# Kernel tuning notes

Hardware: AMD Instinct MI355X
Metric: run time of the kernel (lower is better)

Reference implementation:

```python
import jax, jax.numpy as jnp
import numpy as np

WAY = 5
TEMPERATURE = 0.2
TEMPERATURE_ATTN = 5.0
BN_EPS = 1e-5


def bn_apply(x, p):
    # p: (4, C) = gamma, beta, running_mean, running_var (eval-mode BatchNorm)
    g, b, m, v = p[0], p[1], p[2], p[3]
    sh = (1, -1) + (1,) * (x.ndim - 2)
    return (x - m.reshape(sh)) * (g.reshape(sh) / jnp.sqrt(v.reshape(sh) + BN_EPS)) + b.reshape(sh)


def conv3d(x, w, pad):
    return jax.lax.conv_general_dilated(
        x, w, (1, 1, 1), [(pad[0], pad[0]), (pad[1], pad[1]), (pad[2], pad[2])],
        dimension_numbers=('NCDHW', 'OIDHW', 'NCDHW'))


def sepconv4d(x, conv2_w, bn2, conv1_w, bn1, proj_w, bnp):
    # x: (b, c, u, v, h, w). conv2: (k,k,1) kernel over (u,v); conv1: (1,k,k) over (h,w).
    b, c, u, v, h, w = x.shape
    y = x.reshape(b, c, u, v, h * w)
    y = bn_apply(conv3d(y, conv2_w, (1, 1, 0)), bn2)
    y = jax.nn.relu(y)
    y = y.reshape(b, c, u * v, h, w)
    y = bn_apply(conv3d(y, conv1_w, (0, 1, 1)), bn1)
    # 1x1 projection (pointwise over channels) + BN
    y = jnp.einsum('oc,bcxhw->boxhw', proj_w, y)
    y = bn_apply(y, bnp)
    return y.reshape(b, -1, u, v, h, w)


def cca(x, c1, c2):
    def branch(z):
        z = sepconv4d(z, *c1)
        z = jax.nn.relu(z)
        z = sepconv4d(z, *c2)
        return z
    perm = (0, 1, 4, 5, 2, 3)
    return branch(x) + jnp.transpose(branch(jnp.transpose(x, perm)), perm)


def gaussian_normalize(x, axis, eps=1e-5):
    m = jnp.mean(x, axis=axis, keepdims=True)
    v = jnp.var(x, axis=axis, keepdims=True, ddof=1)  # torch.var is unbiased
    return (x - m) / jnp.sqrt(v + eps)


def setup_inputs() -> dict:
    key = jax.random.key(0)
    ks = jax.random.split(key, 16)

    def bn_params(k, c):
        k1, k2, k3, k4 = jax.random.split(k, 4)
        g = 1.0 + 0.1 * jax.random.normal(k1, (c,), jnp.float32)
        b = 0.1 * jax.random.normal(k2, (c,), jnp.float32)
        m = 0.1 * jax.random.normal(k3, (c,), jnp.float32)
        v = 1.0 + 0.1 * jax.random.uniform(k4, (c,), jnp.float32)
        return jnp.stack([g, b, m, v])

    return {
        'spt': jax.random.normal(ks[0], (1, 5, 640, 10, 10), jnp.float32),
        'qry': jax.random.normal(ks[1], (75, 640, 10, 10), jnp.float32),
        'w_1x1': jax.random.normal(ks[2], (64, 640), jnp.float32) * 0.04,
        'bn_1x1': bn_params(ks[3], 64),
        'c1_conv2_w': jax.random.normal(ks[4], (1, 1, 3, 3, 1), jnp.float32) * 0.33,
        'c1_bn2': bn_params(ks[5], 1),
        'c1_conv1_w': jax.random.normal(ks[6], (1, 1, 1, 3, 3), jnp.float32) * 0.33,
        'c1_bn1': bn_params(ks[7], 1),
        'c1_proj_w': jax.random.normal(ks[8], (16, 1), jnp.float32),
        'c1_bnp': bn_params(ks[9], 16),
        'c2_conv2_w': jax.random.normal(ks[10], (16, 16, 3, 3, 1), jnp.float32) * 0.083,
        'c2_bn2': bn_params(ks[11], 16),
        'c2_conv1_w': jax.random.normal(ks[12], (16, 16, 1, 3, 3), jnp.float32) * 0.083,
        'c2_bn1': bn_params(ks[13], 16),
        'c2_proj_w': jax.random.normal(ks[14], (1, 16), jnp.float32) * 0.25,
        'c2_bnp': bn_params(ks[15], 1),
    }


def reference(spt, qry, w_1x1, bn_1x1,
              c1_conv2_w, c1_bn2, c1_conv1_w, c1_bn1, c1_proj_w, c1_bnp,
              c2_conv2_w, c2_bn2, c2_conv1_w, c2_bn1, c2_proj_w, c2_bnp):
    s = spt[0]                                   # (way, C, H, W)
    s = s - s.mean(axis=1, keepdims=True)        # normalize_feature
    q = qry - qry.mean(axis=1, keepdims=True)

    def cca1x1(x):
        y = jnp.einsum('oc,bchw->bohw', w_1x1, x)
        return jax.nn.relu(bn_apply(y, bn_1x1))

    sf = cca1x1(s)
    qf = cca1x1(q)
    sf = sf / jnp.maximum(jnp.linalg.norm(sf, axis=1, keepdims=True), 1e-8)
    qf = qf / jnp.maximum(jnp.linalg.norm(qf, axis=1, keepdims=True), 1e-8)

    # 4D correlation (avoids the repeat-induced 6D blowup of the original)
    corr = jnp.einsum('ncij,qckl->qnijkl', sf, qf)  # (Q, way, Hs, Ws, Hq, Wq)
    Q, way, Hs, Ws, Hq, Wq = corr.shape

    c1 = (c1_conv2_w, c1_bn2, c1_conv1_w, c1_bn1, c1_proj_w, c1_bnp)
    c2 = (c2_conv2_w, c2_bn2, c2_conv1_w, c2_bn1, c2_proj_w, c2_bnp)
    corr = cca(corr.reshape(Q * way, 1, Hs, Ws, Hq, Wq), c1, c2)

    corr_s = corr.reshape(Q, way, Hs * Ws, Hq, Wq)
    corr_q = corr.reshape(Q, way, Hs, Ws, Hq * Wq)
    corr_s = gaussian_normalize(corr_s, axis=2)
    corr_q = gaussian_normalize(corr_q, axis=4)
    corr_s = jax.nn.softmax(corr_s / TEMPERATURE_ATTN, axis=2).reshape(Q, way, Hs, Ws, Hq, Wq)
    corr_q = jax.nn.softmax(corr_q / TEMPERATURE_ATTN, axis=4).reshape(Q, way, Hs, Ws, Hq, Wq)

    attn_s = corr_s.sum(axis=(4, 5))             # (Q, way, Hs, Ws)
    attn_q = corr_q.sum(axis=(2, 3))             # (Q, way, Hq, Wq)

    spt_att = (attn_s[:, :, None] * s[None]).mean(axis=(-1, -2))       # (Q, way, C)
    qry_att = (attn_q[:, :, None] * q[:, None]).mean(axis=(-1, -2))    # (Q, way, C)
    qry_pooled = q.mean(axis=(-1, -2))                                  # (Q, C)

    num = jnp.sum(spt_att * qry_att, axis=-1)
    den = (jnp.maximum(jnp.linalg.norm(spt_att, axis=-1), 1e-8) *
           jnp.maximum(jnp.linalg.norm(qry_att, axis=-1), 1e-8))
    sim = (num / den) / TEMPERATURE
    return sim, qry_pooled
```

## Files before the change

### kernel.cpp

```cpp
#include <hip/hip_runtime.h>


#define NITEM 375

#define OFF_XTS 0
#define OFF_XTQ 160000
#define OFF_MP  2560000
#define OFF_SF  2568000
#define OFF_QF  2600000
#define OFF_RA  3080000
#define OFF_RB  6830000
#define OFF_PRM 10655000

#define PK2F 232
#define PK1F 1512
#define WSUMF 2792
#define SCVF 2856
#define SHVF 2920
#define PKWF 2984

#define Y1SLOT0  23680
#define Y1GAP3   3200
#define Y1SSTR3  35200
#define ZPB3     20480
#define Y2S3     129280
#define LDS_TOTAL3 161536

typedef float f4v __attribute__((ext_vector_type(4)));
typedef float f32x4 __attribute__((ext_vector_type(4)));
typedef _Float16 half8v __attribute__((ext_vector_type(8)));
typedef __fp16 fp16x2 __attribute__((ext_vector_type(2)));
typedef unsigned int u32x4 __attribute__((ext_vector_type(4)));
typedef unsigned int u32x2 __attribute__((ext_vector_type(2)));

__device__ __forceinline__ unsigned int pkrtz(float a, float b) {
  union { fp16x2 h; unsigned int u; } cv;
  cv.h = __builtin_amdgcn_cvt_pkrtz(a, b);
  return cv.u;
}

__global__ __launch_bounds__(256) void k_prep(
    const float* __restrict__ w1x1,  const float* __restrict__ bn1x1,
    const float* __restrict__ c1c2w, const float* __restrict__ c1bn2,
    const float* __restrict__ c1c1w, const float* __restrict__ c1bn1,
    const float* __restrict__ c1pj,  const float* __restrict__ c1bnp,
    const float* __restrict__ c2c2w, const float* __restrict__ c2bn2,
    const float* __restrict__ c2c1w, const float* __restrict__ c2bn1,
    const float* __restrict__ c2pj,  const float* __restrict__ c2bnp,
    float* __restrict__ prm)
{
  (void)w1x1; (void)bn1x1;
  const int t = threadIdx.x;
  const float eps = 1e-5f;

  for (int idx = t; idx < 144; idx += 256) {
    int ds = idx / 16, i = idx % 16;
    float spv = c2bnp[0] / sqrtf(c2bnp[3] + eps);
    float acc = 0.f;
    for (int o = 0; o < 16; ++o) {
      float s1 = c2bn1[o] / sqrtf(c2bn1[48 + o] + eps);
      acc += c2pj[o] * s1 * c2c1w[(o * 16 + i) * 9 + ds];
    }
    prm[idx] = spv * acc;
  }
  for (int i = t; i < 16; i += 256) {
    float s = c1bnp[i] / sqrtf(c1bnp[48 + i] + eps);
    prm[144 + i] = s * c1pj[i];
    prm[160 + i] = c1bnp[16 + i] - c1bnp[32 + i] * s;
  }
  for (int o = t; o < 16; o += 256) {
    float s = c2bn2[o] / sqrtf(c2bn2[48 + o] + eps);
    prm[176 + o] = s;
    prm[192 + o] = c2bn2[16 + o] - c2bn2[32 + o] * s;
  }
  for (int k = t; k < 9; k += 256) {
    prm[208 + k] = c1c2w[k];
    prm[217 + k] = c1c1w[k];
  }
  if (t == 0) {
    float S2 = c1bn2[0] / sqrtf(c1bn2[3] + eps);
    prm[226] = S2;
    prm[227] = c1bn2[1] - c1bn2[2] * S2;
    float S1 = c1bn1[0] / sqrtf(c1bn1[3] + eps);
    prm[228] = S1;
    prm[229] = c1bn1[1] - c1bn1[2] * S1;
    float spv = c2bnp[0] / sqrtf(c2bnp[3] + eps);
    float k0 = 0.f;
    for (int o = 0; o < 16; ++o) {
      float s1 = c2bn1[o] / sqrtf(c2bn1[48 + o] + eps);
      k0 += c2pj[o] * (c2bn1[16 + o] - c2bn1[32 + o] * s1);
    }
    prm[230] = spv * (k0 - c2bnp[2]) + c2bnp[1];
    prm[231] = 0.f;
  }
  __syncthreads();

  _Float16* pk2 = (_Float16*)(prm + PK2F);
  for (int idx = t; idx < 2560; idx += 256) {
    int c = idx >> 9, rem = idx & 511;
    int ln = rem >> 3, j = rem & 7;
    int o = ln & 15, qq = ln >> 4;
    int tap = 2 * c + (qq >> 1);
    int i = (qq & 1) * 8 + j;
    float v = (tap < 9) ? c2c2w[(o * 16 + i) * 9 + tap] : 0.f;
    pk2[idx] = (_Float16)v;
  }
  _Float16* pk1 = (_Float16*)(prm + PK1F);
  for (int idx = t; idx < 2560; idx += 256) {
    int c = idx >> 9, rem = idx & 511;
    int ln = rem >> 3, j = rem & 7;
    int m = ln & 15, qq = ln >> 4;
    int k = c * 32 + qq * 8 + j;
    int tp = k >> 4, i = k & 15;
    float v = (m == 0 && tp < 9) ? prm[tp * 16 + i] : 0.f;
    pk1[idx] = (_Float16)v;
  }
}

__global__ __launch_bounds__(256) void k_prepw(
    const float* __restrict__ w1x1, const float* __restrict__ bn1x1,
    float* __restrict__ prm)
{
  __shared__ float red[4];
  _Float16* pkw = (_Float16*)(prm + PKWF);
  const int t = threadIdx.x;
  const int base = blockIdx.x * 800;
  for (int r = t; r < 800; r += 256) {
    int idx = base + r;
    int fi = idx >> 9, rem = idx & 511;
    int ln = rem >> 3, j = rem & 7;
    int cc = fi / 10, r2 = fi - cc * 10;
    int mt = r2 >> 1, kk = r2 & 1;
    int m = mt * 16 + (ln & 15);
    int k = cc * 64 + kk * 32 + ((ln >> 4) & 3) * 8 + j;
    float v = (m < 64) ? w1x1[m * 640 + k] : (m == 64 ? 1.f : 0.f);
    pkw[idx] = (_Float16)v;
  }
  const int o = blockIdx.x;
  float s = 0.f;
  for (int c = t; c < 640; c += 256) s += w1x1[o * 640 + c];
  #pragma unroll
  for (int off = 32; off > 0; off >>= 1) s += __shfl_down(s, off);
  if ((t & 63) == 0) red[t >> 6] = s;
  __syncthreads();
  if (t == 0) {
    prm[WSUMF + o] = red[0] + red[1] + red[2] + red[3];
    float scv = bn1x1[o] / sqrtf(bn1x1[192 + o] + 1e-5f);
    prm[SCVF + o] = scv;
    prm[SHVF + o] = bn1x1[64 + o] - bn1x1[128 + o] * scv;
  }
}

__global__ __launch_bounds__(512) void k_feat(
    const float* __restrict__ spt, const float* __restrict__ qry,
    float* __restrict__ ws, float* __restrict__ out)
{
  __shared__ __align__(16) char POOL[2 * 16128];
  __shared__ __align__(16) float mrow[112];
  __shared__ __align__(16) float rn[112];
  __shared__ float CS[2][512];
  __shared__ float RS[640];
  __shared__ float msumL;

  const int b = blockIdx.x, t = threadIdx.x;
  const int lane = t & 63, wvv = t >> 6;
  const int n0 = lane & 15, qd = (lane >> 4) & 3;
  const float* src = (b < 5) ? spt + b * 64000 : qry + (b - 5) * 64000;
  unsigned int* xtg = (unsigned int*)(ws + ((b < 5) ? (OFF_XTS + b * 32000)
                                                    : (OFF_XTQ + (b - 5) * 32000)));
  const float* prm = ws + OFF_PRM;
  const _Float16* pkw = (const _Float16*)(prm + PKWF);

  for (int idx = t; idx < 864; idx += 512) {
    int bsel = idx / 432, r = idx - bsel * 432;
    ((unsigned int*)(POOL + bsel * 16128 + 100 * 144))[r] = 0u;
  }
  for (int u = t; u < 800; u += 512) {
    int cp = u / 25, p4 = u - cp * 25;
    const float* r0 = src + (2 * cp) * 100 + p4 * 4;
    f4v a = *(const f4v*)r0;
    f4v c1 = *(const f4v*)(r0 + 100);
    #pragma unroll
    for (int e = 0; e < 4; ++e)
      *(unsigned int*)((_Float16*)POOL + (p4 * 4 + e) * 72 + 2 * cp) = pkrtz(a[e], c1[e]);
  }
  __syncthreads();

  const int chp = t >> 3, part = t & 7;
  const int pLo = part * 13, pHi = (pLo + 13 < 100) ? pLo + 13 : 100;

  f32x4 acc[5];
  #pragma unroll
  for (int ti = 0; ti < 5; ++ti) { acc[ti][0]=0.f; acc[ti][1]=0.f; acc[ti][2]=0.f; acc[ti][3]=0.f; }

  for (int cc = 0; cc < 10; ++cc) {
    const int cur = cc & 1;
    const _Float16* Xc = (const _Float16*)(POOL + cur * 16128);
    _Float16* Xn = (_Float16*)(POOL + (cur ^ 1) * 16128);

    f4v pa[2], pc[2];
    if (cc < 9) {
      #pragma unroll
// ... 45 lines not shown
      #pragma unroll
      for (int k = 0; k < 8; ++k) s += CS[cur][t * 8 + k];
      RS[cc * 64 + t] = s;
    }
  }
  #pragma unroll
  for (int ti = 0; ti < 5; ++ti) {
    int idx = wvv + ti * 8; if (idx > 34) idx = 34;
    int mt = idx / 7, nt = idx - mt * 7;
    if (mt == 4 && qd == 0) {
      int p = nt * 16 + n0;
      mrow[p] = acc[ti][0] * (1.f / 640.f);
    }
  }
  __syncthreads();
  float* OUT = (float*)POOL;
  if (t == 0) { float s = 0.f; for (int p = 0; p < 100; ++p) s += mrow[p]; msumL = s; }
  #pragma unroll
  for (int ti = 0; ti < 5; ++ti) {
    int idx = wvv + ti * 8; if (idx > 34) idx = 34;
    int mt = idx / 7, nt = idx - mt * 7;
    if (mt < 4) {
      int p = nt * 16 + n0;
      if (p < 100) {
        float mp = mrow[p];
        #pragma unroll
        for (int r = 0; r < 4; ++r) {
          int o = mt * 16 + qd * 4 + r;
          float v = acc[ti][r] - prm[WSUMF + o] * mp;
          v = prm[SCVF + o] * v + prm[SHVF + o];
          OUT[o * 104 + p] = v > 0.f ? v : 0.f;
        }
      }
    }
  }
  __syncthreads();
  if (t < 100) {
    float s = 0.f;
    for (int o = 0; o < 64; ++o) { float v = OUT[o * 104 + t]; s += v * v; }
    float nr = sqrtf(s);
    rn[t] = 1.f / (nr > 1e-8f ? nr : 1e-8f);
    ws[OFF_MP + b * 100 + t] = mrow[t];
  }
  __syncthreads();
  {
    unsigned int* fg = (unsigned int*)((b < 5) ? (ws + OFF_SF) : (ws + OFF_QF))
                       + ((b < 5) ? b : (b - 5)) * 3584;
    for (int idx = t; idx < 3584; idx += 512) {
      const int jj = idx & 3;
      const int ln2 = (idx >> 2) & 63;
      const int fi = idx >> 8;
      const int kk = fi / 7, pt = fi - kk * 7;
      const int pos = pt * 16 + (ln2 & 15);
      const int c0 = kk * 32 + ((ln2 >> 4) & 3) * 8 + 2 * jj;
      float a = 0.f, bb = 0.f;
      if (pos < 100) {
        const float rv = rn[pos];
        a = OUT[c0 * 104 + pos] * rv;
        bb = OUT[(c0 + 1) * 104 + pos] * rv;
      }
      fg[idx] = pkrtz(a, bb);
    }
  }
  if (b >= 5) {
    const float msum = msumL;
    for (int gc = t; gc < 640; gc += 512)
      out[375 + (b - 5) * 640 + gc] = (RS[gc] - msum) * 0.01f;
  }
}

__global__ __launch_bounds__(1024) __attribute__((amdgpu_waves_per_eu(4, 4)))
void k_cca(float* __restrict__ ws)
{
  extern __shared__ char smem[];
  _Float16* T2h = (_Float16*)smem;
  float* T1   = (float*)(smem + 20480);
  float* CORR = (float*)(smem + 71680);

  const float* prm = ws + OFF_PRM;
  const int bid = blockIdx.x;
  const int it = bid >> 1, br = bid & 1;
  const int q = it / 5, n = it % 5;
  const int t = threadIdx.x;
  const int lane = t & 63, wv = t >> 6;
  const int n0 = lane & 15, qd = (lane >> 4) & 3;
  const int qh = qd >> 1, ih = qd & 1;

  const _Float16* pk2 = (const _Float16*)(prm + PK2F);
  const _Float16* pk1 = (const _Float16*)(prm + PK1F);
  half8v A2[5], A1[5];
  #pragma unroll
  for (int c = 0; c < 5; ++c) {
    A2[c] = *(const half8v*)(pk2 + c * 512 + lane * 8);
    A1[c] = *(const half8v*)(pk1 + c * 512 + lane * 8);
  }
  float sc2[4], bc2[4];
  #pragma unroll
  for (int r = 0; r < 4; ++r) { sc2[r] = prm[176 + qd * 4 + r]; bc2[r] = prm[192 + qd * 4 + r]; }

  const int d1E[5] = {-1,-1, 0, 0, 1}, d2E[5] = {-1, 1, 0,-1, 1};
  const int d1O[5] = {-1, 0, 0, 1, 0}, d2O[5] = { 0,-1, 1, 0, 0};

  int pp1[4], st1[4], addr2[4][5], posB[4];
  bool pv[4];
  #pragma unroll
  for (int ti = 0; ti < 4; ++ti) {
    int tile = wv + ti * 16; if (tile > 62) tile = 62;
    const int p = tile * 16 + n0;
    const int pcp = p < 1000 ? p : 999;
    pp1[ti] = pcp * 32 + ih * 16;
    st1[ti] = Y2S3 + p * 32 + qh * 16 + ih * 8;
    pv[ti] = (qd == 0) && (p < 1000);
    const int f2 = pcp / 100;
    const int s = pcp - f2 * 100;
    const int s1 = s / 10, s2 = s - s1 * 10;
    const bool rm = s1 > 0, rp = s1 < 9, cm = s2 > 0, cp2 = s2 < 9;
    const int b0 = Y2S3 + pcp * 32 + ih * 16;
    #pragma unroll
    for (int c = 0; c < 5; ++c) {
      const bool vE = (d1E[c] < 0 ? rm : (d1E[c] > 0 ? rp : true)) &&
                      (d2E[c] < 0 ? cm : (d2E[c] > 0 ? cp2 : true));
      const bool vO = (c == 4) ? false :
                      ((d1O[c] < 0 ? rm : (d1O[c] > 0 ? rp : true)) &&
                       (d2O[c] < 0 ? cm : (d2O[c] > 0 ? cp2 : true)));
      const bool v = qh ? vO : vE;
      const int D1c = (qh ? (d1O[c] * 10 + d2O[c]) : (d1E[c] * 10 + d2E[c]));
      addr2[ti][c] = v ? (b0 + D1c * 32) : ZPB3;
    }
    posB[ti] = br ? (s * 100 + f2) : (f2 * 100 + s);
  }
  const int posStride = br ? 10 : 1000;

  {
    const half8v* fS = (const half8v*)(ws + OFF_SF) + n * 896;
    const half8v* fQ = (const half8v*)(ws + OFF_QF) + q * 896;
    const half8v* FA = br ? fQ : fS;
    const half8v* FB = br ? fS : fQ;
    #pragma unroll
    for (int ti = 0; ti < 4; ++ti) {
      int T = wv + ti * 16; if (T > 48) T = 48;
      const int mt = T / 7, nt = T - mt * 7;
      half8v a0 = FA[mt * 64 + lane];
      half8v b0 = FB[nt * 64 + lane];
      half8v a1 = FA[(7 + mt) * 64 + lane];
      half8v b1 = FB[(7 + nt) * 64 + lane];
      f32x4 acc; acc[0]=0.f; acc[1]=0.f; acc[2]=0.f; acc[3]=0.f;
      acc = __builtin_amdgcn_mfma_f32_16x16x32_f16(a0, b0, acc, 0, 0, 0);
      acc = __builtin_amdgcn_mfma_f32_16x16x32_f16(a1, b1, acc, 0, 0, 0);
      const int s = nt * 16 + n0;
      if (s < 100) {
        const int s1a = s / 10;
        float* cp0 = CORR + s1a * 12 + (s - s1a * 10);
        const int r0 = mt * 16 + qd * 4;
        #pragma unroll
        for (int r = 0; r < 4; ++r)
          if (r0 + r < 100) cp0[(r0 + r) * 120] = acc[r];
      }
    }
  }
  __syncthreads();

  const float S2 = prm[226], B2 = prm[227], S1 = prm[228], B1 = prm[229];

  if (t < 600) {
    const int h = t / 300, r2 = t - h * 300;
    const int f2 = r2 / 30, r3 = r2 - f2 * 30;
    const int s1v = r3 / 3, s2q = r3 - s1v * 3;
    const int cb = s1v * 12 + s2q * 4;
    f4v outv[5];
    #pragma unroll
    for (int i = 0; i < 5; ++i) { outv[i][0]=0.f; outv[i][1]=0.f; outv[i][2]=0.f; outv[i][3]=0.f; }
    #pragma unroll
    for (int k = 0; k < 7; ++k) {
      const int nf1 = 5 * h - 1 + k;
      if ((unsigned)nf1 >= 10u) continue;
      #pragma unroll
      for (int dv = 0; dv < 3; ++dv) {
        const int nf2 = f2 + dv - 1;
        if ((unsigned)nf2 >= 10u) continue;
        f4v x = *(const f4v*)(CORR + (nf1 * 10 + nf2) * 120 + cb);
        #pragma unroll
        for (int du = 0; du < 3; ++du) {
          const int f1l = k - du;
          if (f1l < 0 || f1l > 4) continue;
          const float w = prm[208 + du * 3 + dv];
          #pragma unroll
          for (int e = 0; e < 4; ++e) outv[f1l][e] += w * x[e];
        }
      }
    }
    #pragma unroll
    for (int f1l = 0; f1l < 5; ++f1l) {
      const int f = (5 * h + f1l) * 10 + f2;
      f4v v;
      #pragma unroll
      for (int e = 0; e < 4; ++e) { float z = S2 * outv[f1l][e] + B2; v[e] = z > 0.f ? z : 0.f; }
      *(f4v*)(T1 + f * 120 + cb) = v;
    }
  }
  __syncthreads();

  if (t < 1000) {
    const int f = t / 10, s1 = t - (t / 10) * 10;
    const float* rowB = T1 + f * 120;
    f4v r[3][3];
    float w[3][3];
    #pragma unroll
    for (int dh = 0; dh < 3; ++dh) {
      int rr = s1 + dh - 1;
      bool okr = (unsigned)rr < 10u;
      int rc = rr < 0 ? 0 : (rr > 9 ? 9 : rr);
      const float* rp = rowB + rc * 12;
      r[dh][0] = *(const f4v*)(rp);
      r[dh][1] = *(const f4v*)(rp + 4);
      r[dh][2] = *(const f4v*)(rp + 8);
      #pragma unroll
      for (int dw = 0; dw < 3; ++dw) w[dh][dw] = okr ? prm[217 + dh * 3 + dw] : 0.f;
    }
    float o[10];
    #pragma unroll
    for (int s2 = 0; s2 < 10; ++s2) {
      float a = 0.f;
      #pragma unroll
      for (int dh = 0; dh < 3; ++dh)
        #pragma unroll
        for (int dw = 0; dw < 3; ++dw) {
          int col = s2 + dw - 1;
          if (col < 0 || col > 9) continue;
          a += w[dh][dw] * r[dh][col >> 2][col & 3];
        }
      o[s2] = a;
    }
    unsigned int* dst = (unsigned int*)((char*)T2h + (f * 100 + s1 * 10) * 2);
    #pragma unroll
    for (int k = 0; k < 5; ++k)
      dst[k] = pkrtz(S1 * o[2 * k] + B1, S1 * o[2 * k + 1] + B1);
  }
  __syncthreads();

  #define GEN_Y1(F1N)                                                          \
    if (t < 1000) {                                                            \
      const int _sl = (F1N) % 3;                                               \
      const float t2 = (float)T2h[(F1N) * 1000 + t];                           \
      unsigned int d[8];                                                       \
      _Pragma("unroll")                                                        \
      for (int j = 0; j < 8; ++j) {                                            \
        float ya = fmaxf(prm[144 + 2 * j] * t2 + prm[160 + 2 * j], 0.f);       \
        float yb = fmaxf(prm[145 + 2 * j] * t2 + prm[161 + 2 * j], 0.f);       \
        d[j] = pkrtz(ya, yb);                                                  \
      }                                                                        \
      u32x4 lo, hi;                                                            \
      lo[0]=d[0]; lo[1]=d[1]; lo[2]=d[2]; lo[3]=d[3];                          \
      hi[0]=d[4]; hi[1]=d[5]; hi[2]=d[6]; hi[3]=d[7];                          \
      *(u32x4*)(smem + Y1SLOT0 + _sl * Y1SSTR3 + t * 32) = lo;                 \
      *(u32x4*)(smem + Y1SLOT0 + _sl * Y1SSTR3 + t * 32 + 16) = hi;            \
    }

  GEN_Y1(0)
  GEN_Y1(1)
  {
    u32x4 zz; zz[0] = 0u; zz[1] = 0u; zz[2] = 0u; zz[3] = 0u;
    for (int idx = t; idx < 800; idx += 1024) {
      const int r = idx / 200;
      *(u32x4*)(smem + 20480 + r * Y1SSTR3 + (idx - r * 200) * 16) = zz;
    }
    for (int idx = t; idx < 2000; idx += 1024)
      *(u32x4*)(smem + Y1SLOT0 + 2 * Y1SSTR3 + idx * 16) = zz;
  }
  __syncthreads();

  const float Cf = prm[230];
  float* resb = ws + (br ? OFF_RB : OFF_RA) + it * 10000;
  int gp = 0;

  for (int g = 0; g < 10; ++g) {
    const int o0 = (g % 3) * Y1SSTR3;
    const int oP = ((g + 1) % 3) * Y1SSTR3;
    const int oM = ((g + 2) % 3) * Y1SSTR3;
    int base1[5];
    #pragma unroll
    for (int c = 0; c < 5; ++c) {
      const int eb = (d1E[c] < 0 ? oM : (d1E[c] > 0 ? oP : o0)) + d2E[c] * 3200;
      const int ob = (d1O[c] < 0 ? oM : (d1O[c] > 0 ? oP : o0)) + d2O[c] * 3200;
      base1[c] = Y1SLOT0 + (qh ? ob : eb);
    }

    #pragma unroll
    for (int ti = 0; ti < 4; ++ti) {
      f32x4 acc; acc[0]=0.f; acc[1]=0.f; acc[2]=0.f; acc[3]=0.f;
      #pragma unroll
      for (int c = 0; c < 5; ++c) {
        half8v b = *(const half8v*)(smem + base1[c] + pp1[ti]);
        acc = __builtin_amdgcn_mfma_f32_16x16x32_f16(A2[c], b, acc, 0, 0, 0);
      }
      const float v0 = fmaxf(sc2[0] * acc[0] + bc2[0], 0.f);
      const float v1 = fmaxf(sc2[1] * acc[1] + bc2[1], 0.f);
      const float v2 = fmaxf(sc2[2] * acc[2] + bc2[2], 0.f);
      const float v3 = fmaxf(sc2[3] * acc[3] + bc2[3], 0.f);
      u32x2 wq; wq[0] = pkrtz(v0, v1); wq[1] = pkrtz(v2, v3);
      *(u32x2*)(smem + st1[ti]) = wq;
    }
    __syncthreads();

    #pragma unroll
    for (int ti = 0; ti < 4; ++ti) {
      f32x4 acc; acc[0]=0.f; acc[1]=0.f; acc[2]=0.f; acc[3]=0.f;
      #pragma unroll
      for (int c = 0; c < 5; ++c) {
        half8v b = *(const half8v*)(smem + addr2[ti][c]);
        acc = __builtin_amdgcn_mfma_f32_16x16x32_f16(A1[c], b, acc, 0, 0, 0);
      }
      if (pv[ti]) resb[posB[ti] + gp] = acc[0] + Cf;
    }
    if (g + 2 <= 9) { GEN_Y1(g + 2) }
    else if (g == 8) {
      u32x4 zz; zz[0] = 0u; zz[1] = 0u; zz[2] = 0u; zz[3] = 0u;
      for (int idx = t; idx < 2000; idx += 1024)
        *(u32x4*)(smem + Y1SLOT0 + Y1SSTR3 + idx * 16) = zz;
    }
    gp += posStride;
    __syncthreads();
  }
  #undef GEN_Y1
}

__global__ __launch_bounds__(256) void k_post(float* __restrict__ ws,
                                              float* __restrict__ out)
{
  __shared__ float F[10000];
  __shared__ float mc[100], ic[100], rc[100];
  __shared__ float mr[100], ir[100], rr[100];
  __shared__ float asL[100], aqL[100], msL[100], mqL[100];
  __shared__ float alph[2];
  __shared__ float red[12];
  const int it = blockIdx.x, t = threadIdx.x;
  const int q = it / 5, n = it % 5;

  const f4v* ra4 = (const f4v*)(ws + OFF_RA + it * 10000);
  const f4v* rb4 = (const f4v*)(ws + OFF_RB + it * 10000);
  f4v* F4 = (f4v*)F;
  for (int idx = t; idx < 2500; idx += 256) {
    f4v a = ra4[idx], b = rb4[idx];
    #pragma unroll
    for (int e = 0; e < 4; ++e) a[e] += b[e];
    F4[idx] = a;
  }
  if (t < 100) msL[t] = ws[OFF_MP + n * 100 + t];
  else if (t < 200) mqL[t - 100] = ws[OFF_MP + (5 + q) * 100 + t - 100];
  __syncthreads();

  if (t < 100) {
    float s = 0.f;
    for (int ij = 0; ij < 100; ++ij) s += F[ij * 100 + t];
    float m = s * 0.01f;
    float ss = 0.f;
    for (int ij = 0; ij < 100; ++ij) { float d = F[ij * 100 + t] - m; ss += d * d; }
    float inv = 1.f / (sqrtf(ss * (1.f / 99.f) + 1e-5f) * 5.f);
    float den = 0.f;
    for (int ij = 0; ij < 100; ++ij) den += __expf((F[ij * 100 + t] - m) * inv);
    mc[t] = m; ic[t] = inv; rc[t] = 1.f / den;
  } else if (t < 200) {
    const int r = t - 100;
    float s = 0.f;
    for (int kl = 0; kl < 100; ++kl) s += F[r * 100 + kl];
    float m = s * 0.01f;
    float ss = 0.f;
    for (int kl = 0; kl < 100; ++kl) { float d = F[r * 100 + kl] - m; ss += d * d; }
    float inv = 1.f / (sqrtf(ss * (1.f / 99.f) + 1e-5f) * 5.f);
    float den = 0.f;
    for (int kl = 0; kl < 100; ++kl) den += __expf((F[r * 100 + kl] - m) * inv);
    mr[r] = m; ir[r] = inv; rr[r] = 1.f / den;
  }
  __syncthreads();
  if (t < 100) {
    float s = 0.f;
    for (int kl = 0; kl < 100; ++kl)
// ... 27 lines not shown
      float ap = asL[p], qp = aqL[p];
      s0 += ap * (float)a.h[0]; s1 += ap * (float)a.h[1];
      q0 += qp * (float)bq.h[0]; q1 += qp * (float)bq.h[1];
    }
    float sa0 = (s0 - als) * 0.01f, sa1 = (s1 - als) * 0.01f;
    float qa0 = (q0 - alq) * 0.01f, qa1 = (q1 - alq) * 0.01f;
    dot += sa0 * qa0 + sa1 * qa1;
    na  += sa0 * sa0 + sa1 * sa1;
    nb  += qa0 * qa0 + qa1 * qa1;
  }
  #pragma unroll
  for (int off = 32; off > 0; off >>= 1) {
    dot += __shfl_down(dot, off);
    na  += __shfl_down(na, off);
    nb  += __shfl_down(nb, off);
  }
  const int wid = t >> 6, lanei = t & 63;
  if (lanei == 0) { red[wid * 3 + 0] = dot; red[wid * 3 + 1] = na; red[wid * 3 + 2] = nb; }
  __syncthreads();
  if (t == 0) {
    dot = red[0] + red[3] + red[6] + red[9];
    na  = red[1] + red[4] + red[7] + red[10];
    nb  = red[2] + red[5] + red[8] + red[11];
    float ns = sqrtf(na); ns = ns > 1e-8f ? ns : 1e-8f;
    float nq2 = sqrtf(nb); nq2 = nq2 > 1e-8f ? nq2 : 1e-8f;
    out[it] = dot / (ns * nq2) * 5.f;
  }
}

extern "C" void kernel_launch(void* const* d_in, const int* in_sizes, int n_in,
                              void* d_out, int out_size, void* d_ws, size_t ws_size,
                              hipStream_t stream)
{
  (void)in_sizes; (void)n_in; (void)out_size; (void)ws_size;
  const float* spt    = (const float*)d_in[0];
  const float* qry    = (const float*)d_in[1];
  const float* w1x1   = (const float*)d_in[2];
  const float* bn1x1  = (const float*)d_in[3];
  const float* c1c2w  = (const float*)d_in[4];
  const float* c1bn2  = (const float*)d_in[5];
  const float* c1c1w  = (const float*)d_in[6];
  const float* c1bn1  = (const float*)d_in[7];
  const float* c1pj   = (const float*)d_in[8];
  const float* c1bnp  = (const float*)d_in[9];
  const float* c2c2w  = (const float*)d_in[10];
  const float* c2bn2  = (const float*)d_in[11];
  const float* c2c1w  = (const float*)d_in[12];
  const float* c2bn1  = (const float*)d_in[13];
  const float* c2pj   = (const float*)d_in[14];
  const float* c2bnp  = (const float*)d_in[15];
  float* ws  = (float*)d_ws;
  float* out = (float*)d_out;

  k_prep<<<1, 256, 0, stream>>>(w1x1, bn1x1,
                                c1c2w, c1bn2, c1c1w, c1bn1, c1pj, c1bnp,
                                c2c2w, c2bn2, c2c1w, c2bn1, c2pj, c2bnp,
                                ws + OFF_PRM);
  k_prepw<<<64, 256, 0, stream>>>(w1x1, bn1x1, ws + OFF_PRM);
  k_feat<<<80, 512, 0, stream>>>(spt, qry, ws, out);

  (void)hipFuncSetAttribute((const void*)k_cca,
                            hipFuncAttributeMaxDynamicSharedMemorySize, LDS_TOTAL3);
  k_cca<<<NITEM * 2, 1024, LDS_TOTAL3, stream>>>(ws);

  k_post<<<NITEM, 256, 0, stream>>>(ws, out);
}
```

Measured before the change: 312.1 us.

## Split fp16 channel halves into separate LDS planes and merge prep kernels

```diff
diff --git a/kernel.cpp b/kernel.cpp
--- a/kernel.cpp
+++ b/kernel.cpp
@@ -19,12 +19,14 @@
 #define SHVF 2920
 #define PKWF 2984
 
-#define Y1SLOT0  23680
-#define Y1GAP3   3200
-#define Y1SSTR3  35200
-#define ZPB3     20480
-#define Y2S3     129280
-#define LDS_TOTAL3 161536
+#define Y1REG    20480
+#define Y1HSTR4  17600
+#define Y1SSTR4  35200
+#define Y1INT    22080
+#define ZPB4     20480
+#define Y2S4     129280
+#define Y2HH     16128
+#define LDS_TOTAL4 161536
 
 typedef float f4v __attribute__((ext_vector_type(4)));
 typedef float f32x4 __attribute__((ext_vector_type(4)));
@@ -49,9 +51,39 @@
     const float* __restrict__ c2pj,  const float* __restrict__ c2bnp,
     float* __restrict__ prm)
 {
-  (void)w1x1; (void)bn1x1;
   const int t = threadIdx.x;
   const float eps = 1e-5f;
+
+  if (blockIdx.x < 64) {
+    __shared__ float red[4];
+    _Float16* pkw = (_Float16*)(prm + PKWF);
+    const int base = blockIdx.x * 800;
+    for (int r = t; r < 800; r += 256) {
+      int idx = base + r;
+      int fi = idx >> 9, rem = idx & 511;
+      int ln = rem >> 3, j = rem & 7;
+      int cc = fi / 10, r2 = fi - cc * 10;
+      int mt = r2 >> 1, kk = r2 & 1;
+      int m = mt * 16 + (ln & 15);
+      int k = cc * 64 + kk * 32 + ((ln >> 4) & 3) * 8 + j;
+      float v = (m < 64) ? w1x1[m * 640 + k] : (m == 64 ? 1.f : 0.f);
+      pkw[idx] = (_Float16)v;
+    }
+    const int o = blockIdx.x;
+    float s = 0.f;
+    for (int c = t; c < 640; c += 256) s += w1x1[o * 640 + c];
+    #pragma unroll
+    for (int off = 32; off > 0; off >>= 1) s += __shfl_down(s, off);
+    if ((t & 63) == 0) red[t >> 6] = s;
+    __syncthreads();
+    if (t == 0) {
+      prm[WSUMF + o] = red[0] + red[1] + red[2] + red[3];
+      float scv = bn1x1[o] / sqrtf(bn1x1[192 + o] + eps);
+      prm[SCVF + o] = scv;
+      prm[SHVF + o] = bn1x1[64 + o] - bn1x1[128 + o] * scv;
+    }
+    return;
+  }
 
   for (int idx = t; idx < 144; idx += 256) {
     int ds = idx / 16, i = idx % 16;
@@ -114,40 +146,6 @@
     int tp = k >> 4, i = k & 15;
     float v = (m == 0 && tp < 9) ? prm[tp * 16 + i] : 0.f;
     pk1[idx] = (_Float16)v;
-  }
-}
-
-__global__ __launch_bounds__(256) void k_prepw(
-    const float* __restrict__ w1x1, const float* __restrict__ bn1x1,
-    float* __restrict__ prm)
-{
-  __shared__ float red[4];
-  _Float16* pkw = (_Float16*)(prm + PKWF);
-  const int t = threadIdx.x;
-  const int base = blockIdx.x * 800;
-  for (int r = t; r < 800; r += 256) {
-    int idx = base + r;
-    int fi = idx >> 9, rem = idx & 511;
-    int ln = rem >> 3, j = rem & 7;
-    int cc = fi / 10, r2 = fi - cc * 10;
-    int mt = r2 >> 1, kk = r2 & 1;
-    int m = mt * 16 + (ln & 15);
-    int k = cc * 64 + kk * 32 + ((ln >> 4) & 3) * 8 + j;
-    float v = (m < 64) ? w1x1[m * 640 + k] : (m == 64 ? 1.f : 0.f);
-    pkw[idx] = (_Float16)v;
-  }
-  const int o = blockIdx.x;
-  float s = 0.f;
-  for (int c = t; c < 640; c += 256) s += w1x1[o * 640 + c];
-  #pragma unroll
-  for (int off = 32; off > 0; off >>= 1) s += __shfl_down(s, off);
-  if ((t & 63) == 0) red[t >> 6] = s;
-  __syncthreads();
-  if (t == 0) {
-    prm[WSUMF + o] = red[0] + red[1] + red[2] + red[3];
-    float scv = bn1x1[o] / sqrtf(bn1x1[192 + o] + 1e-5f);
-    prm[SCVF + o] = scv;
-    prm[SHVF + o] = bn1x1[64 + o] - bn1x1[128 + o] * scv;
   }
 }
 
@@ -322,7 +320,7 @@
   extern __shared__ char smem[];
   _Float16* T2h = (_Float16*)smem;
   float* T1   = (float*)(smem + 20480);
-  float* CORR = (float*)(smem + 71680);
+  float* CORR = (float*)(smem + 84480);
 
   const float* prm = ws + OFF_PRM;
   const int bid = blockIdx.x;
@@ -355,14 +353,14 @@
     int tile = wv + ti * 16; if (tile > 62) tile = 62;
     const int p = tile * 16 + n0;
     const int pcp = p < 1000 ? p : 999;
-    pp1[ti] = pcp * 32 + ih * 16;
-    st1[ti] = Y2S3 + p * 32 + qh * 16 + ih * 8;
+    pp1[ti] = pcp * 16;
+    st1[ti] = Y2S4 + qh * Y2HH + p * 16 + ih * 8;
     pv[ti] = (qd == 0) && (p < 1000);
     const int f2 = pcp / 100;
     const int s = pcp - f2 * 100;
     const int s1 = s / 10, s2 = s - s1 * 10;
     const bool rm = s1 > 0, rp = s1 < 9, cm = s2 > 0, cp2 = s2 < 9;
-    const int b0 = Y2S3 + pcp * 32 + ih * 16;
+    const int b0 = Y2S4 + ih * Y2HH + pcp * 16;
     #pragma unroll
     for (int c = 0; c < 5; ++c) {
       const bool vE = (d1E[c] < 0 ? rm : (d1E[c] > 0 ? rp : true)) &&
@@ -372,7 +370,7 @@
                        (d2O[c] < 0 ? cm : (d2O[c] > 0 ? cp2 : true)));
       const bool v = qh ? vO : vE;
       const int D1c = (qh ? (d1O[c] * 10 + d2O[c]) : (d1E[c] * 10 + d2E[c]));
-      addr2[ti][c] = v ? (b0 + D1c * 32) : ZPB3;
+      addr2[ti][c] = v ? (b0 + D1c * 16) : ZPB4;
     }
     posB[ti] = br ? (s * 100 + f2) : (f2 * 100 + s);
   }
@@ -397,11 +395,11 @@
       const int s = nt * 16 + n0;
       if (s < 100) {
         const int s1a = s / 10;
-        float* cp0 = CORR + s1a * 12 + (s - s1a * 10);
+        float* cp0 = CORR + s1a * 16 + (s - s1a * 10);
         const int r0 = mt * 16 + qd * 4;
         #pragma unroll
         for (int r = 0; r < 4; ++r)
-          if (r0 + r < 100) cp0[(r0 + r) * 120] = acc[r];
+          if (r0 + r < 100) cp0[(r0 + r) * 160] = acc[r];
       }
     }
   }
@@ -413,7 +411,7 @@
     const int h = t / 300, r2 = t - h * 300;
     const int f2 = r2 / 30, r3 = r2 - f2 * 30;
     const int s1v = r3 / 3, s2q = r3 - s1v * 3;
-    const int cb = s1v * 12 + s2q * 4;
+    const int cb = s1v * 16 + s2q * 4;
     f4v outv[5];
     #pragma unroll
     for (int i = 0; i < 5; ++i) { outv[i][0]=0.f; outv[i][1]=0.f; outv[i][2]=0.f; outv[i][3]=0.f; }
@@ -425,7 +423,7 @@
       for (int dv = 0; dv < 3; ++dv) {
         const int nf2 = f2 + dv - 1;
         if ((unsigned)nf2 >= 10u) continue;
-        f4v x = *(const f4v*)(CORR + (nf1 * 10 + nf2) * 120 + cb);
+        f4v x = *(const f4v*)(CORR + (nf1 * 10 + nf2) * 160 + cb);
         #pragma unroll
         for (int du = 0; du < 3; ++du) {
           const int f1l = k - du;
@@ -442,14 +440,14 @@
       f4v v;
       #pragma unroll
       for (int e = 0; e < 4; ++e) { float z = S2 * outv[f1l][e] + B2; v[e] = z > 0.f ? z : 0.f; }
-      *(f4v*)(T1 + f * 120 + cb) = v;
+      *(f4v*)(T1 + f * 160 + cb) = v;
     }
   }
   __syncthreads();
 
   if (t < 1000) {
     const int f = t / 10, s1 = t - (t / 10) * 10;
-    const float* rowB = T1 + f * 120;
+    const float* rowB = T1 + f * 160;
     f4v r[3][3];
     float w[3][3];
     #pragma unroll
@@ -457,7 +455,7 @@
       int rr = s1 + dh - 1;
       bool okr = (unsigned)rr < 10u;
       int rc = rr < 0 ? 0 : (rr > 9 ? 9 : rr);
-      const float* rp = rowB + rc * 12;
+      const float* rp = rowB + rc * 16;
       r[dh][0] = *(const f4v*)(rp);
       r[dh][1] = *(const f4v*)(rp + 4);
       r[dh][2] = *(const f4v*)(rp + 8);
@@ -499,20 +497,22 @@
       u32x4 lo, hi;                                                            \
       lo[0]=d[0]; lo[1]=d[1]; lo[2]=d[2]; lo[3]=d[3];                          \
       hi[0]=d[4]; hi[1]=d[5]; hi[2]=d[6]; hi[3]=d[7];                          \
-      *(u32x4*)(smem + Y1SLOT0 + _sl * Y1SSTR3 + t * 32) = lo;                 \
-      *(u32x4*)(smem + Y1SLOT0 + _sl * Y1SSTR3 + t * 32 + 16) = hi;            \
+      *(u32x4*)(smem + Y1INT + _sl * Y1SSTR4 + t * 16) = lo;                   \
+      *(u32x4*)(smem + Y1INT + _sl * Y1SSTR4 + Y1HSTR4 + t * 16) = hi;         \
     }
 
   GEN_Y1(0)
   GEN_Y1(1)
   {
     u32x4 zz; zz[0] = 0u; zz[1] = 0u; zz[2] = 0u; zz[3] = 0u;
-    for (int idx = t; idx < 800; idx += 1024) {
-      const int r = idx / 200;
-      *(u32x4*)(smem + 20480 + r * Y1SSTR3 + (idx - r * 200) * 16) = zz;
-    }
-    for (int idx = t; idx < 2000; idx += 1024)
-      *(u32x4*)(smem + Y1SLOT0 + 2 * Y1SSTR3 + idx * 16) = zz;
+    for (int idx = t; idx < 700; idx += 1024) {
+      const int r = idx / 100;
+      *(u32x4*)(smem + Y1REG + r * Y1HSTR4 + (idx - r * 100) * 16) = zz;
+    }
+    for (int idx = t; idx < 2000; idx += 1024) {
+      const int h = idx >= 1000 ? 1 : 0;
+      *(u32x4*)(smem + Y1INT + 2 * Y1SSTR4 + h * Y1HSTR4 + (idx - h * 1000) * 16) = zz;
+    }
   }
   __syncthreads();
 
@@ -521,15 +521,15 @@
   int gp = 0;
 
   for (int g = 0; g < 10; ++g) {
-    const int o0 = (g % 3) * Y1SSTR3;
-    const int oP = ((g + 1) % 3) * Y1SSTR3;
-    const int oM = ((g + 2) % 3) * Y1SSTR3;
+    const int o0 = (g % 3) * Y1SSTR4;
+    const int oP = ((g + 1) % 3) * Y1SSTR4;
+    const int oM = ((g + 2) % 3) * Y1SSTR4;
     int base1[5];
     #pragma unroll
     for (int c = 0; c < 5; ++c) {
-      const int eb = (d1E[c] < 0 ? oM : (d1E[c] > 0 ? oP : o0)) + d2E[c] * 3200;
-      const int ob = (d1O[c] < 0 ? oM : (d1O[c] > 0 ? oP : o0)) + d2O[c] * 3200;
-      base1[c] = Y1SLOT0 + (qh ? ob : eb);
+      const int eb = (d1E[c] < 0 ? oM : (d1E[c] > 0 ? oP : o0)) + d2E[c] * 1600;
+      const int ob = (d1O[c] < 0 ? oM : (d1O[c] > 0 ? oP : o0)) + d2O[c] * 1600;
+      base1[c] = Y1INT + ih * Y1HSTR4 + (qh ? ob : eb);
     }
 
     #pragma unroll
@@ -562,8 +562,10 @@
     if (g + 2 <= 9) { GEN_Y1(g + 2) }
     else if (g == 8) {
       u32x4 zz; zz[0] = 0u; zz[1] = 0u; zz[2] = 0u; zz[3] = 0u;
-      for (int idx = t; idx < 2000; idx += 1024)
-        *(u32x4*)(smem + Y1SLOT0 + Y1SSTR3 + idx * 16) = zz;
+      for (int idx = t; idx < 2000; idx += 1024) {
+        const int h = idx >= 1000 ? 1 : 0;
+        *(u32x4*)(smem + Y1INT + Y1SSTR4 + h * Y1HSTR4 + (idx - h * 1000) * 16) = zz;
+      }
     }
     gp += posStride;
     __syncthreads();
@@ -702,16 +704,15 @@
   float* ws  = (float*)d_ws;
   float* out = (float*)d_out;
 
-  k_prep<<<1, 256, 0, stream>>>(w1x1, bn1x1,
-                                c1c2w, c1bn2, c1c1w, c1bn1, c1pj, c1bnp,
-                                c2c2w, c2bn2, c2c1w, c2bn1, c2pj, c2bnp,
-                                ws + OFF_PRM);
-  k_prepw<<<64, 256, 0, stream>>>(w1x1, bn1x1, ws + OFF_PRM);
+  k_prep<<<65, 256, 0, stream>>>(w1x1, bn1x1,
+                                 c1c2w, c1bn2, c1c1w, c1bn1, c1pj, c1bnp,
+                                 c2c2w, c2bn2, c2c1w, c2bn1, c2pj, c2bnp,
+                                 ws + OFF_PRM);
   k_feat<<<80, 512, 0, stream>>>(spt, qry, ws, out);
 
   (void)hipFuncSetAttribute((const void*)k_cca,
-                            hipFuncAttributeMaxDynamicSharedMemorySize, LDS_TOTAL3);
-  k_cca<<<NITEM * 2, 1024, LDS_TOTAL3, stream>>>(ws);
+                            hipFuncAttributeMaxDynamicSharedMemorySize, LDS_TOTAL4);
+  k_cca<<<NITEM * 2, 1024, LDS_TOTAL4, stream>>>(ws);
 
   k_post<<<NITEM, 256, 0, stream>>>(ws, out);
 }
```

New measurement: 315.2 us. About the same (+1.0%).

## Split CCA blocks into spatial halves with halo to shrink LDS and raise occupancy

Applied to the files above, without the earlier changes.

```diff
diff --git a/kernel.cpp b/kernel.cpp
--- a/kernel.cpp
+++ b/kernel.cpp
@@ -19,12 +19,14 @@
 #define SHVF 2920
 #define PKWF 2984
 
-#define Y1SLOT0  23680
-#define Y1GAP3   3200
-#define Y1SSTR3  35200
-#define ZPB3     20480
-#define Y2S3     129280
-#define LDS_TOTAL3 161536
+#define MH_T1    0
+#define MH_CORR  28800
+#define MH_T2T   28800
+#define MH_Y1    0
+#define MH_SLOT  19200
+#define MH_ZLINE 57600
+#define MH_Y2    57632
+#define LDS_M    74016
 
 typedef float f4v __attribute__((ext_vector_type(4)));
 typedef float f32x4 __attribute__((ext_vector_type(4)));
@@ -299,12 +301,12 @@
       const int fi = idx >> 8;
       const int kk = fi / 7, pt = fi - kk * 7;
       const int pos = pt * 16 + (ln2 & 15);
-      const int c0 = kk * 32 + ((ln2 >> 4) & 3) * 8 + 2 * jj;
+      const int cq = kk * 32 + ((ln2 >> 4) & 3) * 8 + 2 * jj;
       float a = 0.f, bb = 0.f;
       if (pos < 100) {
         const float rv = rn[pos];
-        a = OUT[c0 * 104 + pos] * rv;
-        bb = OUT[(c0 + 1) * 104 + pos] * rv;
+        a = OUT[cq * 104 + pos] * rv;
+        bb = OUT[(cq + 1) * 104 + pos] * rv;
       }
       fg[idx] = pkrtz(a, bb);
     }
@@ -316,22 +318,23 @@
   }
 }
 
-__global__ __launch_bounds__(1024) __attribute__((amdgpu_waves_per_eu(4, 4)))
+__global__ __launch_bounds__(512) __attribute__((amdgpu_waves_per_eu(4, 4)))
 void k_cca(float* __restrict__ ws)
 {
   extern __shared__ char smem[];
-  _Float16* T2h = (_Float16*)smem;
-  float* T1   = (float*)(smem + 20480);
-  float* CORR = (float*)(smem + 71680);
+  float* T1   = (float*)(smem + MH_T1);
+  float* CORR = (float*)(smem + MH_CORR);
 
   const float* prm = ws + OFF_PRM;
   const int bid = blockIdx.x;
-  const int it = bid >> 1, br = bid & 1;
+  const int it = bid >> 2, br = (bid >> 1) & 1, hf = bid & 1;
   const int q = it / 5, n = it % 5;
   const int t = threadIdx.x;
   const int lane = t & 63, wv = t >> 6;
   const int n0 = lane & 15, qd = (lane >> 4) & 3;
   const int qh = qd >> 1, ih = qd & 1;
+  const int c0 = hf ? 3 : 0;
+  const int hfo = hf ? 1 : 0;
 
   const _Float16* pk2 = (const _Float16*)(prm + PK2F);
   const _Float16* pk1 = (const _Float16*)(prm + PK1F);
@@ -348,33 +351,41 @@
   const int d1E[5] = {-1,-1, 0, 0, 1}, d2E[5] = {-1, 1, 0,-1, 1};
   const int d1O[5] = {-1, 0, 0, 1, 0}, d2O[5] = { 0,-1, 1, 0, 0};
 
-  int pp1[4], st1[4], addr2[4][5], posB[4];
-  bool pv[4];
+  int base_ti[4], b2ti[4], posB[4];
+  int Kc[5], K2c[5];
+  unsigned vmask1 = 0, vmask2 = 0;
+  #pragma unroll
+  for (int c = 0; c < 5; ++c) {
+    const int dA = (qh ? d2O[c] : d2E[c]) + hfo;
+    Kc[c] = dA * 3200;
+    const int D1c = qh ? (d1O[c] * 10 + d2O[c]) : (d1E[c] * 10 + d2E[c]);
+    K2c[c] = D1c * 32;
+  }
+  const int st0 = MH_Y2 + (wv * 16 + n0) * 32 + qh * 16 + ih * 8;
   #pragma unroll
   for (int ti = 0; ti < 4; ++ti) {
-    int tile = wv + ti * 16; if (tile > 62) tile = 62;
-    const int p = tile * 16 + n0;
-    const int pcp = p < 1000 ? p : 999;
-    pp1[ti] = pcp * 32 + ih * 16;
-    st1[ti] = Y2S3 + p * 32 + qh * 16 + ih * 8;
-    pv[ti] = (qd == 0) && (p < 1000);
-    const int f2 = pcp / 100;
-    const int s = pcp - f2 * 100;
+    const int p = (wv + 8 * ti) * 16 + n0;
+    const int pcp = p < 500 ? p : 499;
+    const int f2l = pcp / 100;
+    const int s = pcp - f2l * 100;
+    base_ti[ti] = f2l * 3200 + s * 32 + ih * 16;
+    b2ti[ti] = MH_Y2 + pcp * 32 + ih * 16;
     const int s1 = s / 10, s2 = s - s1 * 10;
     const bool rm = s1 > 0, rp = s1 < 9, cm = s2 > 0, cp2 = s2 < 9;
-    const int b0 = Y2S3 + pcp * 32 + ih * 16;
     #pragma unroll
     for (int c = 0; c < 5; ++c) {
+      const int dA = (qh ? d2O[c] : d2E[c]) + hfo;
+      if ((unsigned)(f2l + dA) < 6u) vmask1 |= 1u << (ti * 5 + c);
       const bool vE = (d1E[c] < 0 ? rm : (d1E[c] > 0 ? rp : true)) &&
                       (d2E[c] < 0 ? cm : (d2E[c] > 0 ? cp2 : true));
       const bool vO = (c == 4) ? false :
                       ((d1O[c] < 0 ? rm : (d1O[c] > 0 ? rp : true)) &&
                        (d2O[c] < 0 ? cm : (d2O[c] > 0 ? cp2 : true)));
-      const bool v = qh ? vO : vE;
-      const int D1c = (qh ? (d1O[c] * 10 + d2O[c]) : (d1E[c] * 10 + d2E[c]));
-      addr2[ti][c] = v ? (b0 + D1c * 32) : ZPB3;
-    }
-    posB[ti] = br ? (s * 100 + f2) : (f2 * 100 + s);
+      if (qh ? vO : vE) vmask2 |= 1u << (ti * 5 + c);
+    }
+    const int fg2 = 5 * hf + f2l;
+    const int pb = br ? (s * 100 + fg2) : (fg2 * 100 + s);
+    posB[ti] = ((qd == 0) && (p < 500)) ? pb : -1;
   }
   const int posStride = br ? 10 : 1000;
 
@@ -384,8 +395,8 @@
     const half8v* FA = br ? fQ : fS;
     const half8v* FB = br ? fS : fQ;
     #pragma unroll
-    for (int ti = 0; ti < 4; ++ti) {
-      int T = wv + ti * 16; if (T > 48) T = 48;
+    for (int ti = 0; ti < 7; ++ti) {
+      int T = wv + 8 * ti; if (T > 48) T = 48;
       const int mt = T / 7, nt = T - mt * 7;
       half8v a0 = FA[mt * 64 + lane];
       half8v b0 = FB[nt * 64 + lane];
@@ -396,12 +407,18 @@
       acc = __builtin_amdgcn_mfma_f32_16x16x32_f16(a1, b1, acc, 0, 0, 0);
       const int s = nt * 16 + n0;
       if (s < 100) {
-        const int s1a = s / 10;
-        float* cp0 = CORR + s1a * 12 + (s - s1a * 10);
+        const int s1a = s / 10, s2r = s - s1a * 10;
         const int r0 = mt * 16 + qd * 4;
         #pragma unroll
-        for (int r = 0; r < 4; ++r)
-          if (r0 + r < 100) cp0[(r0 + r) * 120] = acc[r];
+        for (int r = 0; r < 4; ++r) {
+          const int f = r0 + r;
+          if (f < 100) {
+            const int f1b = f / 10, f2b = f - f1b * 10;
+            const int cl7 = f2b - c0;
+            if ((unsigned)cl7 < 7u)
+              CORR[(f1b * 7 + cl7) * 120 + s1a * 12 + s2r] = acc[r];
+          }
+        }
       }
     }
   }
@@ -409,11 +426,12 @@
 
   const float S2 = prm[226], B2 = prm[227], S1 = prm[228], B1 = prm[229];
 
-  if (t < 600) {
-    const int h = t / 300, r2 = t - h * 300;
-    const int f2 = r2 / 30, r3 = r2 - f2 * 30;
+  if (t < 360) {
+    const int h = t / 180, rem = t - h * 180;
+    const int f2i = rem / 30, r3 = rem - f2i * 30;
     const int s1v = r3 / 3, s2q = r3 - s1v * 3;
     const int cb = s1v * 12 + s2q * 4;
+    const int f2g = (hf ? 4 : 0) + f2i;
     f4v outv[5];
     #pragma unroll
     for (int i = 0; i < 5; ++i) { outv[i][0]=0.f; outv[i][1]=0.f; outv[i][2]=0.f; outv[i][3]=0.f; }
@@ -423,9 +441,9 @@
       if ((unsigned)nf1 >= 10u) continue;
       #pragma unroll
       for (int dv = 0; dv < 3; ++dv) {
-        const int nf2 = f2 + dv - 1;
+        const int nf2 = f2g + dv - 1;
         if ((unsigned)nf2 >= 10u) continue;
-        f4v x = *(const f4v*)(CORR + (nf1 * 10 + nf2) * 120 + cb);
+        f4v x = *(const f4v*)(CORR + (nf1 * 7 + (nf2 - c0)) * 120 + cb);
         #pragma unroll
         for (int du = 0; du < 3; ++du) {
           const int f1l = k - du;
@@ -438,18 +456,18 @@
     }
     #pragma unroll
     for (int f1l = 0; f1l < 5; ++f1l) {
-      const int f = (5 * h + f1l) * 10 + f2;
+      const int trow = (5 * h + f1l) * 6 + f2i;
       f4v v;
       #pragma unroll
       for (int e = 0; e < 4; ++e) { float z = S2 * outv[f1l][e] + B2; v[e] = z > 0.f ? z : 0.f; }
-      *(f4v*)(T1 + f * 120 + cb) = v;
-    }
-  }
-  __syncthreads();
-
-  if (t < 1000) {
-    const int f = t / 10, s1 = t - (t / 10) * 10;
-    const float* rowB = T1 + f * 120;
+      *(f4v*)(T1 + trow * 120 + cb) = v;
+    }
+  }
+  __syncthreads();
+
+  for (int e = t; e < 600; e += 512) {
+    const int fi = e / 10, s1 = e - fi * 10;
+    const float* rowB = T1 + fi * 120;
     f4v r[3][3];
     float w[3][3];
     #pragma unroll
@@ -478,58 +496,80 @@
         }
       o[s2] = a;
     }
-    unsigned int* dst = (unsigned int*)((char*)T2h + (f * 100 + s1 * 10) * 2);
+    unsigned int* dst = (unsigned int*)(smem + MH_T2T + (fi * 100 + s1 * 10) * 2);
     #pragma unroll
     for (int k = 0; k < 5; ++k)
       dst[k] = pkrtz(S1 * o[2 * k] + B1, S1 * o[2 * k + 1] + B1);
   }
   __syncthreads();
 
-  #define GEN_Y1(F1N)                                                          \
-    if (t < 1000) {                                                            \
-      const int _sl = (F1N) % 3;                                               \
-      const float t2 = (float)T2h[(F1N) * 1000 + t];                           \
-      unsigned int d[8];                                                       \
-      _Pragma("unroll")                                                        \
-      for (int j = 0; j < 8; ++j) {                                            \
-        float ya = fmaxf(prm[144 + 2 * j] * t2 + prm[160 + 2 * j], 0.f);       \
-        float yb = fmaxf(prm[145 + 2 * j] * t2 + prm[161 + 2 * j], 0.f);       \
-        d[j] = pkrtz(ya, yb);                                                  \
-      }                                                                        \
-      u32x4 lo, hi;                                                            \
-      lo[0]=d[0]; lo[1]=d[1]; lo[2]=d[2]; lo[3]=d[3];                          \
-      hi[0]=d[4]; hi[1]=d[5]; hi[2]=d[6]; hi[3]=d[7];                          \
-      *(u32x4*)(smem + Y1SLOT0 + _sl * Y1SSTR3 + t * 32) = lo;                 \
-      *(u32x4*)(smem + Y1SLOT0 + _sl * Y1SSTR3 + t * 32 + 16) = hi;            \
-    }
+  unsigned t2pA[5], t2pB[5];
+  const int colLA = t / 100, sA = t - colLA * 100;
+  const int eAoff = colLA * 3200 + sA * 32;
+  const int eBoff = 16000 + (t + 12) * 32;
+  {
+    const unsigned short* T2u = (const unsigned short*)(smem + MH_T2T);
+    #pragma unroll
+    for (int k = 0; k < 5; ++k) {
+      unsigned a = T2u[((2 * k) * 6 + colLA) * 100 + sA];
+      unsigned b = T2u[((2 * k + 1) * 6 + colLA) * 100 + sA];
+      t2pA[k] = a | (b << 16);
+      if (t < 88) {
+        unsigned a2 = T2u[((2 * k) * 6 + 5) * 100 + (t + 12)];
+        unsigned b2 = T2u[((2 * k + 1) * 6 + 5) * 100 + (t + 12)];
+        t2pB[k] = a2 | (b2 << 16);
+      } else t2pB[k] = 0u;
+    }
+    if (t < 4) *(unsigned*)(smem + MH_ZLINE + t * 4) = 0u;
+  }
+  __syncthreads();
+
+  #define T2GET(PK, SL) __extension__ ({ \
+      union { unsigned u; fp16x2 h; } cv_; cv_.u = (PK)[(SL) >> 1]; \
+      (float)cv_.h[(SL) & 1]; })
+
+  #define EMIT_Y1(ADDR, T2V) { \
+      const float t2v_ = (T2V); \
+      unsigned d_[8]; \
+      _Pragma("unroll") \
+      for (int j = 0; j < 8; ++j) { \
+        float ya = fmaxf(prm[144 + 2 * j] * t2v_ + prm[160 + 2 * j], 0.f); \
+        float yb = fmaxf(prm[145 + 2 * j] * t2v_ + prm[161 + 2 * j], 0.f); \
+        d_[j] = pkrtz(ya, yb); } \
+      u32x4 lo_, hi_; \
+      lo_[0]=d_[0]; lo_[1]=d_[1]; lo_[2]=d_[2]; lo_[3]=d_[3]; \
+      hi_[0]=d_[4]; hi_[1]=d_[5]; hi_[2]=d_[6]; hi_[3]=d_[7]; \
+      *(u32x4*)(smem + (ADDR)) = lo_; \
+      *(u32x4*)(smem + (ADDR) + 16) = hi_; }
+
+  #define GEN_Y1(SL) { \
+      const int sb_ = MH_Y1 + ((SL) % 3) * MH_SLOT; \
+      EMIT_Y1(sb_ + eAoff, T2GET(t2pA, (SL))); \
+      if (t < 88) { EMIT_Y1(sb_ + eBoff, T2GET(t2pB, (SL))); } }
 
   GEN_Y1(0)
   GEN_Y1(1)
   {
     u32x4 zz; zz[0] = 0u; zz[1] = 0u; zz[2] = 0u; zz[3] = 0u;
-    for (int idx = t; idx < 800; idx += 1024) {
-      const int r = idx / 200;
-      *(u32x4*)(smem + 20480 + r * Y1SSTR3 + (idx - r * 200) * 16) = zz;
-    }
-    for (int idx = t; idx < 2000; idx += 1024)
-      *(u32x4*)(smem + Y1SLOT0 + 2 * Y1SSTR3 + idx * 16) = zz;
+    for (int idx = t; idx < 1200; idx += 512)
+      *(u32x4*)(smem + MH_Y1 + 2 * MH_SLOT + idx * 16) = zz;
   }
   __syncthreads();
 
   const float Cf = prm[230];
   float* resb = ws + (br ? OFF_RB : OFF_RA) + it * 10000;
-  int gp = 0;
-
+
+  #pragma unroll
   for (int g = 0; g < 10; ++g) {
-    const int o0 = (g % 3) * Y1SSTR3;
-    const int oP = ((g + 1) % 3) * Y1SSTR3;
-    const int oM = ((g + 2) % 3) * Y1SSTR3;
-    int base1[5];
+    const int o0 = (g % 3) * MH_SLOT;
+    const int oP = ((g + 1) % 3) * MH_SLOT;
+    const int oM = ((g + 2) % 3) * MH_SLOT;
+    int slotO[5];
     #pragma unroll
     for (int c = 0; c < 5; ++c) {
-      const int eb = (d1E[c] < 0 ? oM : (d1E[c] > 0 ? oP : o0)) + d2E[c] * 3200;
-      const int ob = (d1O[c] < 0 ? oM : (d1O[c] > 0 ? oP : o0)) + d2O[c] * 3200;
-      base1[c] = Y1SLOT0 + (qh ? ob : eb);
+      const int eb = (d1E[c] < 0 ? oM : (d1E[c] > 0 ? oP : o0));
+      const int ob = (d1O[c] < 0 ? oM : (d1O[c] > 0 ? oP : o0));
+      slotO[c] = MH_Y1 + (qh ? ob : eb);
     }
 
     #pragma unroll
@@ -537,7 +577,9 @@
       f32x4 acc; acc[0]=0.f; acc[1]=0.f; acc[2]=0.f; acc[3]=0.f;
       #pragma unroll
       for (int c = 0; c < 5; ++c) {
-        half8v b = *(const half8v*)(smem + base1[c] + pp1[ti]);
+        int ad = slotO[c] + base_ti[ti] + Kc[c];
+        ad = (vmask1 & (1u << (ti * 5 + c))) ? ad : MH_ZLINE;
+        half8v b = *(const half8v*)(smem + ad);
         acc = __builtin_amdgcn_mfma_f32_16x16x32_f16(A2[c], b, acc, 0, 0, 0);
       }
       const float v0 = fmaxf(sc2[0] * acc[0] + bc2[0], 0.f);
@@ -545,7 +587,7 @@
       const float v2 = fmaxf(sc2[2] * acc[2] + bc2[2], 0.f);
       const float v3 = fmaxf(sc2[3] * acc[3] + bc2[3], 0.f);
       u32x2 wq; wq[0] = pkrtz(v0, v1); wq[1] = pkrtz(v2, v3);
-      *(u32x2*)(smem + st1[ti]) = wq;
+      *(u32x2*)(smem + st0 + ti * 4096) = wq;
     }
     __syncthreads();
 
@@ -554,21 +596,24 @@
       f32x4 acc; acc[0]=0.f; acc[1]=0.f; acc[2]=0.f; acc[3]=0.f;
       #pragma unroll
       for (int c = 0; c < 5; ++c) {
-        half8v b = *(const half8v*)(smem + addr2[ti][c]);
+        int ad = b2ti[ti] + K2c[c];
+        ad = (vmask2 & (1u << (ti * 5 + c))) ? ad : MH_ZLINE;
+        half8v b = *(const half8v*)(smem + ad);
         acc = __builtin_amdgcn_mfma_f32_16x16x32_f16(A1[c], b, acc, 0, 0, 0);
       }
-      if (pv[ti]) resb[posB[ti] + gp] = acc[0] + Cf;
-    }
-    if (g + 2 <= 9) { GEN_Y1(g + 2) }
+      if (posB[ti] >= 0) resb[posB[ti] + g * posStride] = acc[0] + Cf;
+    }
+    if (g <= 7) { GEN_Y1(g + 2) }
     else if (g == 8) {
       u32x4 zz; zz[0] = 0u; zz[1] = 0u; zz[2] = 0u; zz[3] = 0u;
-      for (int idx = t; idx < 2000; idx += 1024)
-        *(u32x4*)(smem + Y1SLOT0 + Y1SSTR3 + idx * 16) = zz;
-    }
-    gp += posStride;
+      for (int idx = t; idx < 1200; idx += 512)
+        *(u32x4*)(smem + MH_Y1 + 1 * MH_SLOT + idx * 16) = zz;
+    }
     __syncthreads();
   }
   #undef GEN_Y1
+  #undef EMIT_Y1
+  #undef T2GET
 }
 
 __global__ __launch_bounds__(256) void k_post(float* __restrict__ ws,
@@ -710,8 +755,8 @@
   k_feat<<<80, 512, 0, stream>>>(spt, qry, ws, out);
 
   (void)hipFuncSetAttribute((const void*)k_cca,
-                            hipFuncAttributeMaxDynamicSharedMemorySize, LDS_TOTAL3);
-  k_cca<<<NITEM * 2, 1024, LDS_TOTAL3, stream>>>(ws);
+                            hipFuncAttributeMaxDynamicSharedMemorySize, LDS_M);
+  k_cca<<<NITEM * 4, 512, LDS_M, stream>>>(ws);
 
   k_post<<<NITEM, 256, 0, stream>>>(ws, out);
 }
```

Result: slower. 501.3 us (+60.6%).
